# Kernel tuning notes

Measured on AMD Instinct MI355X. Metric: run time of the kernel, lower is better.

The kernel has to match this reference:

```python
import jax, jax.numpy as jnp
import numpy as np
import math

B, T, D, H = 4, 2048, 512, 8
HD = D // H
EPS = 1e-5

def _ln(x, g, b):
    mu = jnp.mean(x, axis=-1, keepdims=True)
    var = jnp.var(x, axis=-1, keepdims=True)
    return (x - mu) * jax.lax.rsqrt(var + EPS) * g + b

def _gelu(x):
    return jax.nn.gelu(x, approximate=False)

def setup_inputs() -> dict:
    key = jax.random.key(0)
    ks = jax.random.split(key, 12)
    s = lambda n: 1.0 / math.sqrt(n)
    inp = {
        'x': jax.random.normal(ks[0], (B, T, D), jnp.float32),
        'Wqkv': jax.random.normal(ks[1], (D, 3 * D), jnp.float32) * s(D),
        'bqkv': jnp.zeros((3 * D,), jnp.float32),
        'Wo': jax.random.normal(ks[2], (D, D), jnp.float32) * s(D),
        'bo': jnp.zeros((D,), jnp.float32),
        'ln1_g': jnp.ones((D,), jnp.float32), 'ln1_b': jnp.zeros((D,), jnp.float32),
        'Wsp': jax.random.normal(ks[3], (D, D), jnp.float32) * s(D),
        'bsp': jnp.zeros((D,), jnp.float32),
        'conv_w': jax.random.normal(ks[4], (D, 1, 3), jnp.float32) * s(3),
        'conv_b': jnp.zeros((D,), jnp.float32),
        'Wt1': jax.random.normal(ks[5], (D, 2 * D), jnp.float32) * s(D),
        'bt1': jnp.zeros((2 * D,), jnp.float32),
        'Wt2': jax.random.normal(ks[6], (2 * D, D), jnp.float32) * s(2 * D),
        'bt2': jnp.zeros((D,), jnp.float32),
        'seqln_g': jnp.ones((D,), jnp.float32), 'seqln_b': jnp.zeros((D,), jnp.float32),
        'decay_logit': jnp.float32(2.0),
        'step_size': jnp.float32(0.5),
        'ln2_g': jnp.ones((D,), jnp.float32), 'ln2_b': jnp.zeros((D,), jnp.float32),
        'Wf1': jax.random.normal(ks[7], (D, 4 * D), jnp.float32) * s(D),
        'bf1': jnp.zeros((4 * D,), jnp.float32),
        'Wf2': jax.random.normal(ks[8], (4 * D, D), jnp.float32) * s(4 * D),
        'bf2': jnp.zeros((D,), jnp.float32),
        'ln3_g': jnp.ones((D,), jnp.float32), 'ln3_b': jnp.zeros((D,), jnp.float32),
    }
    return inp

def _forward(x, Wqkv, bqkv, Wo, bo, ln1_g, ln1_b, Wsp, bsp, conv_w, conv_b,
             Wt1, bt1, Wt2, bt2, seqln_g, seqln_b, decay_logit, step_size,
             ln2_g, ln2_b, Wf1, bf1, Wf2, bf2, ln3_g, ln3_b):
    Bx, Tx, Dx = x.shape
    # ---- causal multi-head attention ----
    qkv = x @ Wqkv + bqkv                                  # [B,T,3D]
    q, k, v = jnp.split(qkv, 3, axis=-1)
    resh = lambda t: t.reshape(Bx, Tx, H, HD).transpose(0, 2, 1, 3)  # [B,H,T,hd]
    q, k, v = resh(q), resh(k), resh(v)
    scores = jnp.einsum('bhqd,bhkd->bhqk', q, k) / math.sqrt(HD)
    causal = jnp.tril(jnp.ones((Tx, Tx), bool))
    scores = jnp.where(causal, scores, jnp.float32(-1e30))
    attn = jax.nn.softmax(scores, axis=-1)
    ao = jnp.einsum('bhqk,bhkd->bhqd', attn, v)
    ao = ao.transpose(0, 2, 1, 3).reshape(Bx, Tx, Dx)
    ao = ao @ Wo + bo
    x = _ln(x + ao, ln1_g, ln1_b)
    # ---- decay-mixing branch ----
    seq_in = x @ Wsp + bsp                                 # [B,T,D]
    # causal depthwise conv1d: pad=2 both sides then trim last 2 == left-pad 2
    lhs = seq_in.transpose(0, 2, 1)                        # [B,D,T]
    conv = jax.lax.conv_general_dilated(
        lhs, conv_w, window_strides=(1,), padding=[(2, 0)],
        feature_group_count=Dx, dimension_numbers=('NCH', 'OIH', 'NCH'))
    seq_conv = (conv + conv_b[None, :, None]).transpose(0, 2, 1)  # [B,T,D]
    delta = _gelu(seq_conv @ Wt1 + bt1) @ Wt2 + bt2
    decay = jax.nn.sigmoid(decay_logit)
    pos = jnp.arange(Tx, dtype=jnp.float32)
    dist = pos[:, None] - pos[None, :]                     # [T,T]
    decay_matrix = jnp.where(dist >= 0, decay ** jnp.clip(dist, 0.0), 0.0)
    seq_out = jnp.einsum('qk,bkd->bqd', decay_matrix, delta * step_size)
    seq_out = _ln(seq_out, seqln_g, seqln_b)
    x = _ln(x + seq_out, ln2_g, ln2_b)
    # ---- FFN ----
    ff = _gelu(x @ Wf1 + bf1) @ Wf2 + bf2
    return _ln(x + ff, ln3_g, ln3_b)

def reference(x, Wqkv, bqkv, Wo, bo, ln1_g, ln1_b, Wsp, bsp, conv_w, conv_b,
              Wt1, bt1, Wt2, bt2, seqln_g, seqln_b, decay_logit, step_size,
              ln2_g, ln2_b, Wf1, bf1, Wf2, bf2, ln3_g, ln3_b):
    return _forward(x, Wqkv, bqkv, Wo, bo, ln1_g, ln1_b, Wsp, bsp, conv_w, conv_b,
                    Wt1, bt1, Wt2, bt2, seqln_g, seqln_b, decay_logit, step_size,
                    ln2_g, ln2_b, Wf1, bf1, Wf2, bf2, ln3_g, ln3_b)
```

## Files before the change

### kernel.cpp

```cpp
#include <hip/hip_runtime.h>
#include <math.h>
#include <type_traits>

typedef __bf16 bf16_t;
typedef __bf16 bf16x8 __attribute__((ext_vector_type(8)));
typedef __bf16 bf16x4 __attribute__((ext_vector_type(4)));
typedef float  f32x4  __attribute__((ext_vector_type(4)));

#define DEVI static __device__ __forceinline__

typedef __attribute__((address_space(1))) void gvoid;
typedef __attribute__((address_space(3))) void lvoid;

DEVI bf16_t f2bf(float f) {
    unsigned u = __builtin_bit_cast(unsigned, f);
    u += 0x7fffu + ((u >> 16) & 1u);
    unsigned short s = (unsigned short)(u >> 16);
    return __builtin_bit_cast(bf16_t, s);
}
DEVI float gelu_f(float x) { return 0.5f * x * (1.0f + erff(x * 0.7071067811865476f)); }

__global__ __launch_bounds__(256)
void k_transpose_cvt(const float* __restrict__ in, bf16_t* __restrict__ out, int K, int N) {
    __shared__ float t[32][33];
    const int n0 = blockIdx.x * 32, k0 = blockIdx.y * 32;
    const int tx = threadIdx.x, ty = threadIdx.y;
    for (int i = ty; i < 32; i += 8)
        t[i][tx] = in[(size_t)(k0 + i) * N + n0 + tx];
    __syncthreads();
    for (int i = ty; i < 32; i += 8)
        out[(size_t)(n0 + i) * K + k0 + tx] = f2bf(t[tx][i]);
}

__global__ __launch_bounds__(256)
void k_cvt(const float* __restrict__ in, bf16_t* __restrict__ out, int n) {
    const int i = (blockIdx.x * 256 + threadIdx.x) * 8;
    if (i >= n) return;
    float4 a = *(const float4*)(in + i);
    float4 b = *(const float4*)(in + i + 4);
    bf16x8 o = { f2bf(a.x), f2bf(a.y), f2bf(a.z), f2bf(a.w),
                 f2bf(b.x), f2bf(b.y), f2bf(b.z), f2bf(b.w) };
    *(bf16x8*)(out + i) = o;
}

template<int OUTMODE>
__global__ __launch_bounds__(256)
void k_gemm(const bf16_t* __restrict__ A, int lda, const bf16_t* __restrict__ Bt, int ldb,
            const float* __restrict__ bias, float* __restrict__ Cf0, float* __restrict__ Cf1,
            bf16_t* __restrict__ Cb, int M, int N, int K) {
    __shared__ __align__(16) bf16_t As[2][4096];
    __shared__ __align__(16) bf16_t Bs[2][4096];
    A  += (size_t)blockIdx.z * K;
    Bt += (size_t)blockIdx.z * K;
    float* __restrict__ Cf = blockIdx.z ? Cf1 : Cf0;

    const int tid = threadIdx.x;
    const int wave = tid >> 6, lane = tid & 63;
    const int lg = lane >> 4, l15 = lane & 15;
    const int m0 = blockIdx.y << 7, n0 = blockIdx.x << 7;
    const int wr = (wave >> 1) * 64, wc = (wave & 1) * 64;

    f32x4 acc[4][4] = {};

    auto stage = [&](int buf, int k0) {
#pragma unroll
        for (int j = 0; j < 2; j++) {
            const int seg = j * 4 + wave;
            const int e = seg * 512 + lane * 8;
            const int r = e >> 5, c = e & 31;
            __builtin_amdgcn_global_load_lds(
                (gvoid*)(A + (size_t)(m0 + r) * lda + k0 + c),
                (lvoid*)(As[buf] + seg * 512), 16, 0, 0);
            __builtin_amdgcn_global_load_lds(
                (gvoid*)(Bt + (size_t)(n0 + r) * ldb + k0 + c),
                (lvoid*)(Bs[buf] + seg * 512), 16, 0, 0);
        }
    };

    const int nk = K >> 5;
    stage(0, 0);
    for (int kt = 0; kt < nk; ++kt) {
        const int cur = kt & 1;
        if (kt + 1 < nk) stage(cur ^ 1, (kt + 1) << 5);
        __syncthreads();
        bf16x8 af[4], bfr[4];
#pragma unroll
        for (int i = 0; i < 4; i++) {
            af[i]  = *(const bf16x8*)(As[cur] + (wr + i * 16 + l15) * 32 + lg * 8);
            bfr[i] = *(const bf16x8*)(Bs[cur] + (wc + i * 16 + l15) * 32 + lg * 8);
        }
#pragma unroll
        for (int i = 0; i < 4; i++)
#pragma unroll
            for (int j = 0; j < 4; j++)
                acc[i][j] = __builtin_amdgcn_mfma_f32_16x16x32_bf16(af[i], bfr[j], acc[i][j], 0, 0, 0);
        __syncthreads();
    }

#pragma unroll
    for (int i = 0; i < 4; i++) {
        const int row0 = m0 + wr + i * 16 + lg * 4;
#pragma unroll
        for (int j = 0; j < 4; j++) {
            const int col = n0 + wc + j * 16 + l15;
            const float bs = bias ? bias[col] : 0.f;
#pragma unroll
            for (int r = 0; r < 4; r++) {
                float v = acc[i][j][r] + bs;
                if (OUTMODE == 2) v = gelu_f(v);
                const size_t idx = (size_t)(row0 + r) * N + col;
                if (OUTMODE == 0) Cf[idx] = v;
                else              Cb[idx] = f2bf(v);
            }
        }
    }
}

__global__ __launch_bounds__(256)
void k_attn(const bf16_t* __restrict__ qkv, bf16_t* __restrict__ ao) {
    const int bh = blockIdx.x;
    const int b = bh >> 3, h = bh & 7;
    const int qi = 31 - (int)blockIdx.y;
    const int q0 = qi << 6;
    const int tid = threadIdx.x;
    const int wave = tid >> 6, lane = tid & 63;
    const int lg = lane >> 4, l15 = lane & 15;

    __shared__ __align__(16) bf16_t Ks[64 * 64];
    __shared__ __align__(16) bf16_t Vt[64 * 64];
    __shared__ __align__(16) bf16_t Ps[64 * 64];

    const bf16_t* __restrict__ qb = qkv + ((size_t)b * 2048) * 1536 + h * 64;
    const bf16_t* __restrict__ kb = qb + 512;
    const bf16_t* __restrict__ vb = qb + 1024;

    const int qrb = q0 + wave * 16;

    bf16x8 qf[2];
#pragma unroll
    for (int c = 0; c < 2; c++)
        qf[c] = *(const bf16x8*)(qb + (size_t)(qrb + l15) * 1536 + c * 32 + lg * 8);

    f32x4 oacc[4] = {};
    float mrun[4], lrun[4];
#pragma unroll
    for (int r = 0; r < 4; r++) { mrun[r] = -3.0e38f; lrun[r] = 0.f; }

    const float SC = 0.125f * 1.44269504088896f;
    const int ntile = qi + 1;

    for (int kt = 0; kt < ntile; ++kt) {
        const int k0 = kt << 6;
#pragma unroll
        for (int it = 0; it < 2; ++it) {
            const int e = (it * 256 + tid) * 8;
            const int tr = e >> 6, tc = e & 63;
            bf16x8 kv = *(const bf16x8*)(kb + (size_t)(k0 + tr) * 1536 + tc);
            bf16x8 vv = *(const bf16x8*)(vb + (size_t)(k0 + tr) * 1536 + tc);
            *(bf16x8*)(Ks + tr * 64 + (tc ^ ((tr & 7) << 3))) = kv;
#pragma unroll
            for (int j = 0; j < 8; j++) {
                const int d = tc + j;
                Vt[d * 64 + (tr ^ ((d & 7) << 3))] = vv[j];
            }
        }
        __syncthreads();

        f32x4 sacc[4] = {};
#pragma unroll
        for (int j = 0; j < 4; j++) {
            const int trow = j * 16 + l15;
#pragma unroll
            for (int c = 0; c < 2; c++) {
                bf16x8 kf = *(const bf16x8*)(Ks + trow * 64 + ((c * 32 + lg * 8) ^ ((trow & 7) << 3)));
                sacc[j] = __builtin_amdgcn_mfma_f32_16x16x32_bf16(qf[c], kf, sacc[j], 0, 0, 0);
            }
        }

        auto smax = [&](auto DIAGC) {
            constexpr bool DIAG = DIAGC.value;
#pragma unroll
            for (int r = 0; r < 4; r++) {
                const int qg = qrb + lg * 4 + r;
                float s[4];
#pragma unroll
                for (int j = 0; j < 4; j++) {
                    float v = sacc[j][r] * SC;
                    if (DIAG) {
                        const int kg = k0 + j * 16 + l15;
                        v = (kg <= qg) ? v : -3.0e38f;
                    }
                    s[j] = v;
                }
                float v = fmaxf(fmaxf(s[0], s[1]), fmaxf(s[2], s[3]));
                v = fmaxf(v, __shfl_xor(v, 1));
                v = fmaxf(v, __shfl_xor(v, 2));
                v = fmaxf(v, __shfl_xor(v, 4));
                v = fmaxf(v, __shfl_xor(v, 8));
                const float mnew = fmaxf(mrun[r], v);
                const float sc = exp2f(mrun[r] - mnew);
                mrun[r] = mnew;
                lrun[r] *= sc;
#pragma unroll
                for (int df = 0; df < 4; df++) oacc[df][r] *= sc;
                const int ql = wave * 16 + lg * 4 + r;
#pragma unroll
                for (int j = 0; j < 4; j++) {
                    const float p = exp2f(s[j] - mnew);
                    lrun[r] += p;
                    Ps[ql * 64 + ((j * 16 + l15) ^ ((ql & 7) << 3))] = f2bf(p);
                }
            }
        };
        if (kt == ntile - 1) smax(std::integral_constant<bool, true>{});
        else                 smax(std::integral_constant<bool, false>{});

#pragma unroll
        for (int kc = 0; kc < 2; kc++) {
            const int ql2 = wave * 16 + l15;
            bf16x8 pa = *(const bf16x8*)(Ps + ql2 * 64 + ((kc * 32 + lg * 8) ^ ((ql2 & 7) << 3)));
#pragma unroll
            for (int df = 0; df < 4; df++) {
                const int d = df * 16 + l15;
                bf16x8 vf = *(const bf16x8*)(Vt + d * 64 + ((kc * 32 + lg * 8) ^ ((d & 7) << 3)));
                oacc[df] = __builtin_amdgcn_mfma_f32_16x16x32_bf16(pa, vf, oacc[df], 0, 0, 0);
            }
        }
        __syncthreads();
    }

#pragma unroll
    for (int r = 0; r < 4; r++) {
        float l = lrun[r];
        l += __shfl_xor(l, 1); l += __shfl_xor(l, 2);
        l += __shfl_xor(l, 4); l += __shfl_xor(l, 8);
        lrun[r] = 1.0f / l;
    }
    bf16_t* __restrict__ aob = ao + ((size_t)b * 2048) * 512 + h * 64;
#pragma unroll
    for (int df = 0; df < 4; df++) {
        const int d = df * 16 + l15;
#pragma unroll
        for (int r = 0; r < 4; r++) {
            const int q = qrb + lg * 4 + r;
            aob[(size_t)q * 512 + d] = f2bf(oacc[df][r] * lrun[r]);
        }
    }
}

DEVI void red2(float& a, float& b, float* sh) {
#pragma unroll
    for (int m = 1; m < 64; m <<= 1) { a += __shfl_xor(a, m); b += __shfl_xor(b, m); }
    const int wv = threadIdx.x >> 6, ln = threadIdx.x & 63;
    __syncthreads();
    if (ln == 0) { sh[wv * 2] = a; sh[wv * 2 + 1] = b; }
    __syncthreads();
    a = sh[0] + sh[2];
    b = sh[1] + sh[3];
}

template<bool WB>
__global__ __launch_bounds__(128)
void k_ln_add(const float* __restrict__ xa, const float* __restrict__ p0,
              const float* __restrict__ p1, const float* __restrict__ bias,
              const float* __restrict__ g, const float* __restrict__ be,
              float* __restrict__ outf, bf16_t* __restrict__ outb) {
    __shared__ float sh[4];
    const int row = blockIdx.x, tid = threadIdx.x;
    const size_t base = (size_t)row * 512 + tid * 4;
    float4 a = *(const float4*)(xa + base);
    float4 b = *(const float4*)(p0 + base);
    float sx = a.x + b.x, sy = a.y + b.y, sz = a.z + b.z, sw = a.w + b.w;
    if (p1) {
        float4 c = *(const float4*)(p1 + base);
        sx += c.x; sy += c.y; sz += c.z; sw += c.w;
    }
    if (bias) {
        float4 c = *(const float4*)(bias + tid * 4);
        sx += c.x; sy += c.y; sz += c.z; sw += c.w;
    }
    float sm = sx + sy + sz + sw;
    float sq = sx * sx + sy * sy + sz * sz + sw * sw;
    red2(sm, sq, sh);
    const float mean = sm * (1.f / 512.f);
    const float var = sq * (1.f / 512.f) - mean * mean;
    const float rs = rsqrtf(var + 1e-5f);
    float4 gv = *(const float4*)(g + tid * 4);
    float4 bv = *(const float4*)(be + tid * 4);
    float4 o;
    o.x = (sx - mean) * rs * gv.x + bv.x;
    o.y = (sy - mean) * rs * gv.y + bv.y;
    o.z = (sz - mean) * rs * gv.z + bv.z;
    o.w = (sw - mean) * rs * gv.w + bv.w;
    *(float4*)(outf + base) = o;
    if (WB) {
        bf16x4 ob = { f2bf(o.x), f2bf(o.y), f2bf(o.z), f2bf(o.w) };
        *(bf16x4*)(outb + base) = ob;
    }
}

__global__ __launch_bounds__(128)
void k_ln_seq(const float* __restrict__ sqo, const float* __restrict__ x1,
              const float* __restrict__ sg, const float* __restrict__ sb,
              const float* __restrict__ g2, const float* __restrict__ b2,
              float* __restrict__ outf, bf16_t* __restrict__ outb) {
    __shared__ float sh[4];
    const int row = blockIdx.x, tid = threadIdx.x;
    const size_t base = (size_t)row * 512 + tid * 4;
    float4 v = *(const float4*)(sqo + base);
    float sm = v.x + v.y + v.z + v.w;
    float sq = v.x * v.x + v.y * v.y + v.z * v.z + v.w * v.w;
    red2(sm, sq, sh);
    float mean = sm * (1.f / 512.f);
    float var = sq * (1.f / 512.f) - mean * mean;
    float rs = rsqrtf(var + 1e-5f);
    float4 sgv = *(const float4*)(sg + tid * 4);
    float4 sbv = *(const float4*)(sb + tid * 4);
    float4 x1v = *(const float4*)(x1 + base);
    float ux = x1v.x + (v.x - mean) * rs * sgv.x + sbv.x;
    float uy = x1v.y + (v.y - mean) * rs * sgv.y + sbv.y;
    float uz = x1v.z + (v.z - mean) * rs * sgv.z + sbv.z;
    float uw = x1v.w + (v.w - mean) * rs * sgv.w + sbv.w;
    float sm2 = ux + uy + uz + uw;
    float sq2 = ux * ux + uy * uy + uz * uz + uw * uw;
    red2(sm2, sq2, sh);
    float mean2 = sm2 * (1.f / 512.f);
    float var2 = sq2 * (1.f / 512.f) - mean2 * mean2;
    float rs2 = rsqrtf(var2 + 1e-5f);
    float4 g2v = *(const float4*)(g2 + tid * 4);
    float4 b2v = *(const float4*)(b2 + tid * 4);
    float4 o;
    o.x = (ux - mean2) * rs2 * g2v.x + b2v.x;
    o.y = (uy - mean2) * rs2 * g2v.y + b2v.y;
    o.z = (uz - mean2) * rs2 * g2v.z + b2v.z;
    o.w = (uw - mean2) * rs2 * g2v.w + b2v.w;
    *(float4*)(outf + base) = o;
    bf16x4 ob = { f2bf(o.x), f2bf(o.y), f2bf(o.z), f2bf(o.w) };
    *(bf16x4*)(outb + base) = ob;
}

__global__ __launch_bounds__(256)
void k_conv(const float* __restrict__ s0, const float* __restrict__ s1,
            const float* __restrict__ bsp, const float* __restrict__ cw,
            const float* __restrict__ cb, bf16_t* __restrict__ out) {
    const int idx = blockIdx.x * 256 + threadIdx.x;
    const int d4 = idx & 127, t = (idx >> 7) & 2047, b = idx >> 18;
    const int d = d4 * 4;
    const size_t base = ((size_t)(b * 2048 + t)) * 512 + d;
    float4 bi = *(const float4*)(bsp + d);
    float a0[4], a1[4] = {0, 0, 0, 0}, a2[4] = {0, 0, 0, 0};
    {
        float4 u = *(const float4*)(s0 + base);
        float4 v = *(const float4*)(s1 + base);
        a0[0] = u.x + v.x + bi.x; a0[1] = u.y + v.y + bi.y;
        a0[2] = u.z + v.z + bi.z; a0[3] = u.w + v.w + bi.w;
    }
    if (t >= 1) {
        float4 u = *(const float4*)(s0 + base - 512);
        float4 v = *(const float4*)(s1 + base - 512);
        a1[0] = u.x + v.x + bi.x; a1[1] = u.y + v.y + bi.y;
        a1[2] = u.z + v.z + bi.z; a1[3] = u.w + v.w + bi.w;
    }
    if (t >= 2) {
        float4 u = *(const float4*)(s0 + base - 1024);
        float4 v = *(const float4*)(s1 + base - 1024);
        a2[0] = u.x + v.x + bi.x; a2[1] = u.y + v.y + bi.y;
        a2[2] = u.z + v.z + bi.z; a2[3] = u.w + v.w + bi.w;
    }
    bf16x4 ob;
#pragma unroll
    for (int e = 0; e < 4; e++) {
        const float w0 = cw[(d + e) * 3 + 0];
        const float w1 = cw[(d + e) * 3 + 1];
        const float w2 = cw[(d + e) * 3 + 2];
        const float v = w2 * a0[e] + w1 * a1[e] + w0 * a2[e] + cb[d + e];
        ob[e] = f2bf(v);
    }
    *(bf16x4*)(out + base) = ob;
}

DEVI float sigm(float x) { return 1.f / (1.f + expf(-x)); }

__global__ __launch_bounds__(256)
void k_scan_local(float* __restrict__ d0, const float* __restrict__ d1,
                  const float* __restrict__ bias, float* __restrict__ tot,
                  const float* __restrict__ dl, const float* __restrict__ ss) {
    const int id = blockIdx.x * 256 + threadIdx.x;
    const int d = id & 511, c = (id >> 9) & 15, b = id >> 13;
    const float dec = sigm(dl[0]), st = ss[0];
    const float bd = bias[d];
    const size_t base = ((size_t)(b * 2048 + c * 128)) * 512 + d;
    float s = 0.f;
    for (int t = 0; t < 128; t++) {
        const size_t off = base + (size_t)t * 512;
        s = dec * s + st * (d0[off] + d1[off] + bd);
        d0[off] = s;
    }
    tot[id] = s;
}

__global__ __launch_bounds__(256)
void k_scan_carry(float* __restrict__ tot, const float* __restrict__ dl) {
    const int id = blockIdx.x * 256 + threadIdx.x;
    const int d = id & 511, b = id >> 9;
    const float dec = sigm(dl[0]);
    const float dec128 = powf(dec, 128.f);
    float carry = 0.f;
    for (int c = 0; c < 16; c++) {
        const size_t i = (size_t)(b * 16 + c) * 512 + d;
        const float t = tot[i];
        tot[i] = carry;
        carry = carry * dec128 + t;
    }
}

__global__ __launch_bounds__(256)
void k_scan_apply(float* __restrict__ x, const float* __restrict__ tot,
                  const float* __restrict__ dl) {
    const int id = blockIdx.x * 256 + threadIdx.x;
    const int d = id & 511, c = (id >> 9) & 15, b = id >> 13;
    const float dec = sigm(dl[0]);
    const float carry = tot[(size_t)(b * 16 + c) * 512 + d];
    float* p = x + ((size_t)(b * 2048 + c * 128)) * 512 + d;
    float f = dec;
    for (int t = 0; t < 128; t++) {
        p[(size_t)t * 512] += carry * f;
        f *= dec;
    }
}

extern "C" void kernel_launch(void* const* d_in, const int* in_sizes, int n_in,
                              void* d_out, int out_size, void* d_ws, size_t ws_size,
                              hipStream_t stream) {
    const float* x     = (const float*)d_in[0];
    const float* Wqkv  = (const float*)d_in[1];
    const float* bqkv  = (const float*)d_in[2];
    const float* Wo    = (const float*)d_in[3];
    const float* bo    = (const float*)d_in[4];
    const float* ln1_g = (const float*)d_in[5];
    const float* ln1_b = (const float*)d_in[6];
    const float* Wsp   = (const float*)d_in[7];
    const float* bsp   = (const float*)d_in[8];
    const float* convw = (const float*)d_in[9];
    const float* convb = (const float*)d_in[10];
    const float* Wt1   = (const float*)d_in[11];
    const float* bt1   = (const float*)d_in[12];
    const float* Wt2   = (const float*)d_in[13];
    const float* bt2   = (const float*)d_in[14];
    const float* sln_g = (const float*)d_in[15];
    const float* sln_b = (const float*)d_in[16];
    const float* dlog  = (const float*)d_in[17];
    const float* sstep = (const float*)d_in[18];
    const float* ln2_g = (const float*)d_in[19];
    const float* ln2_b = (const float*)d_in[20];
    const float* Wf1   = (const float*)d_in[21];
    const float* bf1   = (const float*)d_in[22];
    const float* Wf2   = (const float*)d_in[23];
    const float* bf2   = (const float*)d_in[24];
    const float* ln3_g = (const float*)d_in[25];
    const float* ln3_b = (const float*)d_in[26];

    char* ws = (char*)d_ws;
    size_t off = 0;
    auto alloc = [&](size_t bytes) -> void* {
        void* p = ws + off;
        off += (bytes + 255) & ~(size_t)255;
        return p;
    };
    bf16_t* Wqkv_t = (bf16_t*)alloc((size_t)1536 * 512 * 2);
    bf16_t* Wo_t   = (bf16_t*)alloc((size_t)512 * 512 * 2);
    bf16_t* Wsp_t  = (bf16_t*)alloc((size_t)512 * 512 * 2);
    bf16_t* Wt1_t  = (bf16_t*)alloc((size_t)1024 * 512 * 2);
    bf16_t* Wt2_t  = (bf16_t*)alloc((size_t)512 * 1024 * 2);
    bf16_t* Wf1_t  = (bf16_t*)alloc((size_t)2048 * 512 * 2);
    bf16_t* Wf2_t  = (bf16_t*)alloc((size_t)512 * 2048 * 2);
    bf16_t* actb   = (bf16_t*)alloc((size_t)8192 * 512 * 2);
    bf16_t* big    = (bf16_t*)alloc((size_t)8192 * 2048 * 2);
    bf16_t* aob    = (bf16_t*)alloc((size_t)8192 * 512 * 2);
    float*  bufA   = (float*)alloc((size_t)8192 * 512 * 4);
    float*  X1     = (float*)alloc((size_t)8192 * 512 * 4);
    float*  carry  = (float*)alloc((size_t)4 * 16 * 512 * 4);

    float* P1a = (float*)big;
    float* P1b = (float*)(big + (size_t)8192 * 1024);

    const dim3 tb(32, 8);
    k_transpose_cvt<<<dim3(48, 16), tb, 0, stream>>>(Wqkv, Wqkv_t, 512, 1536);
    k_transpose_cvt<<<dim3(16, 16), tb, 0, stream>>>(Wo,   Wo_t,   512, 512);
    k_transpose_cvt<<<dim3(16, 16), tb, 0, stream>>>(Wsp,  Wsp_t,  512, 512);
    k_transpose_cvt<<<dim3(32, 16), tb, 0, stream>>>(Wt1,  Wt1_t,  512, 1024);
    k_transpose_cvt<<<dim3(16, 32), tb, 0, stream>>>(Wt2,  Wt2_t,  1024, 512);
    k_transpose_cvt<<<dim3(64, 16), tb, 0, stream>>>(Wf1,  Wf1_t,  512, 2048);
    k_transpose_cvt<<<dim3(16, 64), tb, 0, stream>>>(Wf2,  Wf2_t,  2048, 512);

    k_cvt<<<2048, 256, 0, stream>>>(x, actb, 8192 * 512);

    k_gemm<1><<<dim3(12, 64, 1), 256, 0, stream>>>(actb, 512, Wqkv_t, 512, bqkv,
                                                   nullptr, nullptr, big, 8192, 1536, 512);
    k_attn<<<dim3(32, 32), 256, 0, stream>>>(big, aob);
    k_gemm<0><<<dim3(4, 64, 2), 256, 0, stream>>>(aob, 512, Wo_t, 512, nullptr,
                                                  bufA, P1a, nullptr, 8192, 512, 256);
    k_ln_add<true><<<8192, 128, 0, stream>>>(x, bufA, P1a, bo, ln1_g, ln1_b, X1, actb);
    k_gemm<0><<<dim3(4, 64, 2), 256, 0, stream>>>(actb, 512, Wsp_t, 512, nullptr,
                                                  bufA, P1a, nullptr, 8192, 512, 256);
    k_conv<<<4096, 256, 0, stream>>>(bufA, P1a, bsp, convw, convb, aob);
    k_gemm<2><<<dim3(8, 64, 1), 256, 0, stream>>>(aob, 512, Wt1_t, 512, bt1,
                                                  nullptr, nullptr, big, 8192, 1024, 512);
    k_gemm<0><<<dim3(4, 64, 2), 256, 0, stream>>>(big, 1024, Wt2_t, 1024, nullptr,
                                                  bufA, P1b, nullptr, 8192, 512, 512);
    k_scan_local<<<128, 256, 0, stream>>>(bufA, P1b, bt2, carry, dlog, sstep);
    k_scan_carry<<<8, 256, 0, stream>>>(carry, dlog);
    k_scan_apply<<<128, 256, 0, stream>>>(bufA, carry, dlog);
    k_ln_seq<<<8192, 128, 0, stream>>>(bufA, X1, sln_g, sln_b, ln2_g, ln2_b, X1, actb);
    k_gemm<2><<<dim3(16, 64, 1), 256, 0, stream>>>(actb, 512, Wf1_t, 512, bf1,
                                                   nullptr, nullptr, big, 8192, 2048, 512);
    k_gemm<0><<<dim3(4, 64, 1), 256, 0, stream>>>(big, 2048, Wf2_t, 2048, bf2,
                                                  bufA, nullptr, nullptr, 8192, 512, 2048);
    k_ln_add<false><<<8192, 128, 0, stream>>>(X1, bufA, nullptr, nullptr, ln3_g, ln3_b,
                                              (float*)d_out, nullptr);
}
```

Measured before the change: 503.6 us.

## Pretranspose V, vectorize P stores, fuse scan apply into LN, split-K FFN2

Adds a separate kernel that transposes V to a global [D,T] layout so attention loads Vt rows with vector loads instead of scattered scalar LDS stores. K rows are permuted so each lane's score columns are contiguous, which lets P be written as one bf16x4 store. The scan carry application moves into the seq LayerNorm kernel, removing a strided pass over the buffer. The FFN down-projection uses split-K into a second buffer when workspace allows, with the bias add folded into the final LN. The cost is an extra transpose kernel, extra workspace, and extra partial-buffer traffic.

After: 455.9 us. 9.5% less time.

```diff
diff --git a/kernel.cpp b/kernel.cpp
--- a/kernel.cpp
+++ b/kernel.cpp
@@ -30,6 +30,20 @@
     __syncthreads();
     for (int i = ty; i < 32; i += 8)
         out[(size_t)(n0 + i) * K + k0 + tx] = f2bf(t[tx][i]);
+}
+
+__global__ __launch_bounds__(256)
+void k_vtrans(const bf16_t* __restrict__ qkv, bf16_t* __restrict__ vtg) {
+    __shared__ bf16_t t[32][33];
+    const int t0 = blockIdx.x * 32, d0 = blockIdx.y * 32, b = blockIdx.z;
+    const int tx = threadIdx.x, ty = threadIdx.y;
+    const bf16_t* src = qkv + ((size_t)b * 2048) * 1536 + 1024;
+    for (int i = ty; i < 32; i += 8)
+        t[i][tx] = src[(size_t)(t0 + i) * 1536 + d0 + tx];
+    __syncthreads();
+    bf16_t* dst = vtg + ((size_t)b * 512) * 2048;
+    for (int i = ty; i < 32; i += 8)
+        dst[(size_t)(d0 + i) * 2048 + t0 + tx] = t[tx][i];
 }
 
 __global__ __launch_bounds__(256)
@@ -117,7 +131,8 @@
 }
 
 __global__ __launch_bounds__(256)
-void k_attn(const bf16_t* __restrict__ qkv, bf16_t* __restrict__ ao) {
+void k_attn(const bf16_t* __restrict__ qkv, const bf16_t* __restrict__ vtg,
+            bf16_t* __restrict__ ao) {
     const int bh = blockIdx.x;
     const int b = bh >> 3, h = bh & 7;
     const int qi = 31 - (int)blockIdx.y;
@@ -132,7 +147,7 @@
 
     const bf16_t* __restrict__ qb = qkv + ((size_t)b * 2048) * 1536 + h * 64;
     const bf16_t* __restrict__ kb = qb + 512;
-    const bf16_t* __restrict__ vb = qb + 1024;
+    const bf16_t* __restrict__ vtb = vtg + ((size_t)(b * 512 + h * 64)) * 2048;
 
     const int qrb = q0 + wave * 16;
 
@@ -154,15 +169,12 @@
 #pragma unroll
         for (int it = 0; it < 2; ++it) {
             const int e = (it * 256 + tid) * 8;
-            const int tr = e >> 6, tc = e & 63;
-            bf16x8 kv = *(const bf16x8*)(kb + (size_t)(k0 + tr) * 1536 + tc);
-            bf16x8 vv = *(const bf16x8*)(vb + (size_t)(k0 + tr) * 1536 + tc);
-            *(bf16x8*)(Ks + tr * 64 + (tc ^ ((tr & 7) << 3))) = kv;
-#pragma unroll
-            for (int j = 0; j < 8; j++) {
-                const int d = tc + j;
-                Vt[d * 64 + (tr ^ ((d & 7) << 3))] = vv[j];
-            }
+            const int rr = e >> 6, cc = e & 63;
+            bf16x8 kv = *(const bf16x8*)(kb + (size_t)(k0 + rr) * 1536 + cc);
+            const int p = (rr & 3) * 16 + (rr >> 2);
+            *(bf16x8*)(Ks + p * 64 + (cc ^ ((p & 7) << 3))) = kv;
+            bf16x8 vv = *(const bf16x8*)(vtb + (size_t)rr * 2048 + k0 + cc);
+            *(bf16x8*)(Vt + rr * 64 + (cc ^ ((rr & 7) << 3))) = vv;
         }
         __syncthreads();
 
@@ -187,7 +199,7 @@
                 for (int j = 0; j < 4; j++) {
                     float v = sacc[j][r] * SC;
                     if (DIAG) {
-                        const int kg = k0 + j * 16 + l15;
+                        const int kg = k0 + l15 * 4 + j;
                         v = (kg <= qg) ? v : -3.0e38f;
                     }
                     s[j] = v;
@@ -204,12 +216,14 @@
 #pragma unroll
                 for (int df = 0; df < 4; df++) oacc[df][r] *= sc;
                 const int ql = wave * 16 + lg * 4 + r;
+                bf16x4 pk;
 #pragma unroll
                 for (int j = 0; j < 4; j++) {
                     const float p = exp2f(s[j] - mnew);
                     lrun[r] += p;
-                    Ps[ql * 64 + ((j * 16 + l15) ^ ((ql & 7) << 3))] = f2bf(p);
+                    pk[j] = f2bf(p);
                 }
+                *(bf16x4*)(Ps + ql * 64 + ((l15 * 4) ^ ((ql & 7) << 3))) = pk;
             }
         };
         if (kt == ntile - 1) smax(std::integral_constant<bool, true>{});
@@ -299,15 +313,24 @@
     }
 }
 
+DEVI float sigm(float x) { return 1.f / (1.f + expf(-x)); }
+
 __global__ __launch_bounds__(128)
-void k_ln_seq(const float* __restrict__ sqo, const float* __restrict__ x1,
+void k_ln_seq(const float* __restrict__ sqo, const float* __restrict__ carry,
+              const float* __restrict__ dl, const float* __restrict__ x1,
               const float* __restrict__ sg, const float* __restrict__ sb,
               const float* __restrict__ g2, const float* __restrict__ b2,
               float* __restrict__ outf, bf16_t* __restrict__ outb) {
     __shared__ float sh[4];
     const int row = blockIdx.x, tid = threadIdx.x;
     const size_t base = (size_t)row * 512 + tid * 4;
+    const int bb = row >> 11, t = row & 2047;
+    const int chunk = t >> 7, tl = t & 127;
+    const float dec = sigm(dl[0]);
+    const float fpow = exp2f(log2f(dec) * (float)(tl + 1));
+    float4 cv = *(const float4*)(carry + (size_t)(bb * 16 + chunk) * 512 + tid * 4);
     float4 v = *(const float4*)(sqo + base);
+    v.x += cv.x * fpow; v.y += cv.y * fpow; v.z += cv.z * fpow; v.w += cv.w * fpow;
     float sm = v.x + v.y + v.z + v.w;
     float sq = v.x * v.x + v.y * v.y + v.z * v.z + v.w * v.w;
     red2(sm, sq, sh);
@@ -379,8 +402,6 @@
     *(bf16x4*)(out + base) = ob;
 }
 
-DEVI float sigm(float x) { return 1.f / (1.f + expf(-x)); }
-
 __global__ __launch_bounds__(256)
 void k_scan_local(float* __restrict__ d0, const float* __restrict__ d1,
                   const float* __restrict__ bias, float* __restrict__ tot,
@@ -411,21 +432,6 @@
         const float t = tot[i];
         tot[i] = carry;
         carry = carry * dec128 + t;
-    }
-}
-
-__global__ __launch_bounds__(256)
-void k_scan_apply(float* __restrict__ x, const float* __restrict__ tot,
-                  const float* __restrict__ dl) {
-    const int id = blockIdx.x * 256 + threadIdx.x;
-    const int d = id & 511, c = (id >> 9) & 15, b = id >> 13;
-    const float dec = sigm(dl[0]);
-    const float carry = tot[(size_t)(b * 16 + c) * 512 + d];
-    float* p = x + ((size_t)(b * 2048 + c * 128)) * 512 + d;
-    float f = dec;
-    for (int t = 0; t < 128; t++) {
-        p[(size_t)t * 512] += carry * f;
-        f *= dec;
     }
 }
 
@@ -477,9 +483,14 @@
     bf16_t* actb   = (bf16_t*)alloc((size_t)8192 * 512 * 2);
     bf16_t* big    = (bf16_t*)alloc((size_t)8192 * 2048 * 2);
     bf16_t* aob    = (bf16_t*)alloc((size_t)8192 * 512 * 2);
+    bf16_t* vtg    = (bf16_t*)alloc((size_t)4 * 512 * 2048 * 2);
     float*  bufA   = (float*)alloc((size_t)8192 * 512 * 4);
     float*  X1     = (float*)alloc((size_t)8192 * 512 * 4);
     float*  carry  = (float*)alloc((size_t)4 * 16 * 512 * 4);
+
+    float* P1c = nullptr;
+    if (ws_size >= off + (size_t)8192 * 512 * 4)
+        P1c = (float*)alloc((size_t)8192 * 512 * 4);
 
     float* P1a = (float*)big;
     float* P1b = (float*)(big + (size_t)8192 * 1024);
@@ -497,7 +508,8 @@
 
     k_gemm<1><<<dim3(12, 64, 1), 256, 0, stream>>>(actb, 512, Wqkv_t, 512, bqkv,
                                                    nullptr, nullptr, big, 8192, 1536, 512);
-    k_attn<<<dim3(32, 32), 256, 0, stream>>>(big, aob);
+    k_vtrans<<<dim3(64, 16, 4), tb, 0, stream>>>(big, vtg);
+    k_attn<<<dim3(32, 32), 256, 0, stream>>>(big, vtg, aob);
     k_gemm<0><<<dim3(4, 64, 2), 256, 0, stream>>>(aob, 512, Wo_t, 512, nullptr,
                                                   bufA, P1a, nullptr, 8192, 512, 256);
     k_ln_add<true><<<8192, 128, 0, stream>>>(x, bufA, P1a, bo, ln1_g, ln1_b, X1, actb);
@@ -510,12 +522,19 @@
                                                   bufA, P1b, nullptr, 8192, 512, 512);
     k_scan_local<<<128, 256, 0, stream>>>(bufA, P1b, bt2, carry, dlog, sstep);
     k_scan_carry<<<8, 256, 0, stream>>>(carry, dlog);
-    k_scan_apply<<<128, 256, 0, stream>>>(bufA, carry, dlog);
-    k_ln_seq<<<8192, 128, 0, stream>>>(bufA, X1, sln_g, sln_b, ln2_g, ln2_b, X1, actb);
+    k_ln_seq<<<8192, 128, 0, stream>>>(bufA, carry, dlog, X1, sln_g, sln_b,
+                                       ln2_g, ln2_b, X1, actb);
     k_gemm<2><<<dim3(16, 64, 1), 256, 0, stream>>>(actb, 512, Wf1_t, 512, bf1,
                                                    nullptr, nullptr, big, 8192, 2048, 512);
-    k_gemm<0><<<dim3(4, 64, 1), 256, 0, stream>>>(big, 2048, Wf2_t, 2048, bf2,
-                                                  bufA, nullptr, nullptr, 8192, 512, 2048);
-    k_ln_add<false><<<8192, 128, 0, stream>>>(X1, bufA, nullptr, nullptr, ln3_g, ln3_b,
-                                              (float*)d_out, nullptr);
-}
+    if (P1c) {
+        k_gemm<0><<<dim3(4, 64, 2), 256, 0, stream>>>(big, 2048, Wf2_t, 2048, nullptr,
+                                                      bufA, P1c, nullptr, 8192, 512, 1024);
+        k_ln_add<false><<<8192, 128, 0, stream>>>(X1, bufA, P1c, bf2, ln3_g, ln3_b,
+                                                  (float*)d_out, nullptr);
+    } else {
+        k_gemm<0><<<dim3(4, 64, 1), 256, 0, stream>>>(big, 2048, Wf2_t, 2048, bf2,
+                                                      bufA, nullptr, nullptr, 8192, 512, 2048);
+        k_ln_add<false><<<8192, 128, 0, stream>>>(X1, bufA, nullptr, nullptr, ln3_g, ln3_b,
+                                                  (float*)d_out, nullptr);
+    }
+}
```
